# Optimization experiments

Hardware: AMD Instinct MI355X
Metric: run time of the kernel (lower is better)

## Reference

```python
import jax, jax.numpy as jnp
import numpy as np
from jax import lax

B, C, H, W = 16, 256, 56, 56
GROUPS = 4
K = 3
DILATIONS = (1, 3, 5)
EPS = 1e-5


@jax.custom_vjp
def bin_act(x):
    return jnp.sign(x)

def _bin_act_fwd(x):
    return jnp.sign(x), x

def _bin_act_bwd(x, g):
    grad = jnp.where((x >= -1.0) & (x <= 0.0), 2.0 + 2.0 * x, 0.0) \
         + jnp.where((x > 0.0) & (x <= 1.0), 2.0 - 2.0 * x, 0.0)
    return (grad * g,)

bin_act.defvjp(_bin_act_fwd, _bin_act_bwd)


def _bin_weight(wi):
    # per-output-channel scaling from raw |w|, centered sign, clip-STE
    scale = lax.stop_gradient(jnp.mean(jnp.abs(wi), axis=(1, 2, 3), keepdims=True))
    wc = wi - jnp.mean(wi, axis=(1, 2, 3), keepdims=True)
    clipped = jnp.clip(wc, -1.0, 1.0)
    return lax.stop_gradient(scale * jnp.sign(wc) - clipped) + clipped


def setup_inputs() -> dict:
    key = jax.random.key(0)
    ks = jax.random.split(key, 3)
    x = jax.random.normal(ks[0], (B, C, H, W), dtype=jnp.float32)
    # 3 branches of grouped conv weights: (3, C_out, C_in/groups, K, K)
    w = jax.random.normal(ks[1], (3, C, C // GROUPS, K, K), dtype=jnp.float32) * 0.05
    cb = jax.random.normal(ks[2], (3, C), dtype=jnp.float32) * 0.01
    return {
        "x": x,
        "bias": jnp.zeros((1, C, 1, 1), jnp.float32),   # LearnableBias
        "w": w,
        "cb": cb,                                        # conv biases
        "move1": jnp.zeros((3, C), jnp.float32),
        "alpha": jnp.full((3, C), 0.25, jnp.float32),    # PReLU slopes
        "move2": jnp.zeros((3, C), jnp.float32),
        "gamma": jnp.ones((C,), jnp.float32),            # LayerNorm weight
        "beta": jnp.zeros((C,), jnp.float32),            # LayerNorm bias
    }


def reference(x, bias, w, cb, move1, alpha, move2, gamma, beta):
    xb = x + bias
    xq = bin_act(xb)  # binarized activations, shared across branches
    out = jnp.zeros_like(x)
    for i, d in enumerate(DILATIONS):
        wq = _bin_weight(w[i])
        y = lax.conv_general_dilated(
            xq, wq,
            window_strides=(1, 1),
            padding=[(d, d), (d, d)],  # 'same' for k=3 with dilation d
            rhs_dilation=(d, d),
            dimension_numbers=("NCHW", "OIHW", "NCHW"),
            feature_group_count=GROUPS,
        )
        y = y + cb[i][None, :, None, None]
        # RPReLU: shift, channel-wise PReLU, shift
        y = y - move1[i][None, :, None, None]
        y = jnp.where(y >= 0, y, alpha[i][None, :, None, None] * y)
        y = y + move2[i][None, :, None, None]
        out = out + y
    # LayerNorm over channel dim (equivalent to NHWC last-dim LN)
    mean = jnp.mean(out, axis=1, keepdims=True)
    var = jnp.var(out, axis=1, keepdims=True)
    out = (out - mean) * lax.rsqrt(var + EPS)
    out = out * gamma[None, :, None, None] + beta[None, :, None, None]
    return out
```

## Files before the change

kernel.cpp:

```cpp
#include <hip/hip_runtime.h>
#include <hip/hip_fp16.h>
#include <stdint.h>

static constexpr int Bc = 16, Cc = 256, Hc = 56, Wc = 56, Gc = 4, CGc = 64;
static constexpr int HWc = Hc * Wc;
static constexpr float EPSc = 1e-5f;


static constexpr int SBS = 260;

__global__ __launch_bounds__(256) void k_prep(
    const float* __restrict__ w, const float* __restrict__ x,
    const float* __restrict__ bias, uint64_t* __restrict__ wbits,
    float* __restrict__ scales, uint64_t* __restrict__ abits,
    uint32_t* __restrict__ zero_area) {
  const int t = threadIdx.x;
  if (blockIdx.x < 192) {
    const int io = blockIdx.x * 4 + (t >> 6);
    const int i = io >> 8, o = io & 255;
    const int lane = t & 63;
    const float* wp = w + (size_t)io * 576 + lane * 9;
    float v[9];
    float ssum = 0.f, sabs = 0.f;
#pragma unroll
    for (int k = 0; k < 9; ++k) {
      v[k] = wp[k];
      ssum += v[k];
      sabs += fabsf(v[k]);
    }
#pragma unroll
    for (int off = 32; off > 0; off >>= 1) {
      ssum += __shfl_down(ssum, off);
      sabs += __shfl_down(sabs, off);
    }
    const float mean = __shfl(ssum, 0) * (1.f / 576.f);
    const float scale = __shfl(sabs, 0) * (1.f / 576.f);
#pragma unroll
    for (int k = 0; k < 9; ++k) {
      unsigned long long m = __ballot(v[k] > mean);
      if (lane == 0) wbits[(i * 9 + k) * Cc + o] = m;
    }
    if (lane == 0) scales[io] = scale;
  } else if (blockIdx.x == 192) {
    zero_area[t] = 0;
  } else {
    __shared__ uint8_t sb[Wc * SBS];
    const int bid = blockIdx.x - 193;
    const int b = bid / Hc, h = bid % Hc;
    const float* xb = x + ((size_t)b * Cc) * HWc + h * Wc;
#pragma unroll
    for (int k = 0; k < 14; ++k) {
      const int idx = k * 256 + t;
      const int c = idx / 14, q = idx - c * 14;
      const float4 v = *(const float4*)(xb + (size_t)c * HWc + q * 4);
      const float bc = bias[c];
      sb[(q * 4 + 0) * SBS + c] = (v.x + bc > 0.f);
      sb[(q * 4 + 1) * SBS + c] = (v.y + bc > 0.f);
      sb[(q * 4 + 2) * SBS + c] = (v.z + bc > 0.f);
      sb[(q * 4 + 3) * SBS + c] = (v.w + bc > 0.f);
    }
    __syncthreads();
    if (t < Gc * Wc) {
      const int g = t / Wc, ww = t - g * Wc;
      const uint32_t* p = (const uint32_t*)(sb + ww * SBS + g * 64);
      uint64_t word = 0;
#pragma unroll
      for (int dw = 0; dw < 16; ++dw) {
        const uint32_t d = p[dw];
        const uint32_t nib = (d | (d >> 7) | (d >> 14) | (d >> 21)) & 0xF;
        word |= (uint64_t)nib << (4 * dw);
      }
      abits[(((size_t)b * Gc + g) * Hc + h) * Wc + ww] = word;
    }
  }
}

template <int D>
struct Branch {
  uint64_t wgt[9];
  const uint64_t *r0, *r1, *r2;
  int BL, BM, BR;
  float sc, cbm1, al;

  __device__ __forceinline__ void init(const uint64_t* __restrict__ wb,
                                       const uint64_t* rowbase,
                                       const uint64_t* zrow, int h,
                                       float sc_, float cbm1_, float al_) {
    sc = sc_; cbm1 = cbm1_; al = al_;
    int z[9];
#pragma unroll
    for (int k = 0; k < 9; ++k) {
      wgt[k] = wb[k * Cc];
      z[k] = 64 - 2 * (int)__builtin_popcountll(wgt[k]);
    }
    const bool v0 = (h - D >= 0), v2 = (h + D < Hc);
    r0 = v0 ? (rowbase + (size_t)(h - D) * Wc) : zrow;
    r1 = rowbase + (size_t)h * Wc;
    r2 = v2 ? (rowbase + (size_t)(h + D) * Wc) : zrow;
    const int Z0 = (v0 ? 0 : z[0]) + (v2 ? 0 : z[6]);
    const int Z1 = (v0 ? 0 : z[1]) + (v2 ? 0 : z[7]);
    const int Z2 = (v0 ? 0 : z[2]) + (v2 ? 0 : z[8]);
    BM = 576 - Z0 - Z1 - Z2;
    BL = 384 - Z1 - Z2;
    BR = 384 - Z0 - Z1;
  }

  __device__ __forceinline__ void accum(int c0, int acc[14]) const {
#pragma unroll
    for (int kh = 0; kh < 3; ++kh) {
      const uint64_t* rp = (kh == 0) ? r0 : (kh == 1 ? r1 : r2);
      uint64_t sa[14 + 2 * D];
#pragma unroll
      for (int j = 0; j < 14 + 2 * D; ++j) sa[j] = rp[c0 - D + j];
#pragma unroll
      for (int ww = 0; ww < 14; ++ww) {
#pragma unroll
        for (int kw = 0; kw < 3; ++kw) {
          const int col = c0 + ww + D * (kw - 1);
          if (col < 0 || col >= Wc) continue;
          acc[ww] += (int)__builtin_popcountll(wgt[kh * 3 + kw] ^ sa[ww + D * kw]);
        }
      }
    }
  }

  __device__ __forceinline__ void epi(int c0, const int acc[14],
                                      float outf[14]) const {
#pragma unroll
    for (int ww = 0; ww < 14; ++ww) {
      const int wg = c0 + ww;
      const int B = (wg < D) ? BL : ((wg >= Wc - D) ? BR : BM);
      const float y0 = fmaf(sc, (float)(B - 2 * acc[ww]), cbm1);
      outf[ww] += fmaxf(y0, 0.f) + al * fminf(y0, 0.f);
    }
  }
};

static constexpr int TS2 = 58;

__global__ __launch_bounds__(256, 4) void k_conv_ln(
    const uint64_t* __restrict__ abits, const uint64_t* __restrict__ zrow,
    const uint64_t* __restrict__ wbits, const float* __restrict__ scales,
    const float* __restrict__ cb, const float* __restrict__ mv1,
    const float* __restrict__ al, const float* __restrict__ mv2,
    const float* __restrict__ gamma, const float* __restrict__ beta,
    float* __restrict__ out) {
  __shared__ __half out_tile[Cc * TS2];
  __shared__ float redu[4][Wc], redq[4][Wc];
  __shared__ float mstat[Wc], rstat[Wc];

  const int bid = blockIdx.x;
  const int b = bid / Hc, h = bid % Hc;
  const int t = threadIdx.x;
  const int gu = __builtin_amdgcn_readfirstlane(t >> 6);

  const uint64_t* rowbase = abits + ((size_t)b * Gc + gu) * Hc * Wc;

  Branch<1> b0; Branch<3> b1; Branch<5> b2;
  b0.init(wbits + 0 * 9 * Cc + t, rowbase, zrow, h, scales[0 * Cc + t],
          cb[0 * Cc + t] - mv1[0 * Cc + t], al[0 * Cc + t]);
  b1.init(wbits + 1 * 9 * Cc + t, rowbase, zrow, h, scales[1 * Cc + t],
          cb[1 * Cc + t] - mv1[1 * Cc + t], al[1 * Cc + t]);
  b2.init(wbits + 2 * 9 * Cc + t, rowbase, zrow, h, scales[2 * Cc + t],
          cb[2 * Cc + t] - mv1[2 * Cc + t], al[2 * Cc + t]);
  const float m2sum = mv2[0 * Cc + t] + mv2[1 * Cc + t] + mv2[2 * Cc + t];

#pragma unroll
  for (int ch = 0; ch < 4; ++ch) {
    const int c0 = ch * 14;
    float outf[14];
#pragma unroll
    for (int ww = 0; ww < 14; ++ww) outf[ww] = m2sum;
    { int acc[14] = {}; b0.accum(c0, acc); b0.epi(c0, acc, outf); }
    { int acc[14] = {}; b1.accum(c0, acc); b1.epi(c0, acc, outf); }
    { int acc[14] = {}; b2.accum(c0, acc); b2.epi(c0, acc, outf); }
#pragma unroll
    for (int ww = 0; ww < 14; ww += 2) {
      __half2 hv;
      hv.x = __float2half(outf[ww]);
      hv.y = __float2half(outf[ww + 1]);
      *(__half2*)&out_tile[t * TS2 + c0 + ww] = hv;
    }
  }
  __syncthreads();

  if (t < 4 * Wc) {
    const int ww = t % Wc;
    const int cq = t / Wc;
    float s = 0.f, sq = 0.f;
#pragma unroll 4
    for (int c = cq * 64; c < cq * 64 + 64; ++c) {
      const float v = __half2float(out_tile[c * TS2 + ww]);
      s += v;
      sq = fmaf(v, v, sq);
    }
    redu[cq][ww] = s;
    redq[cq][ww] = sq;
  }
  __syncthreads();
  if (t < Wc) {
    const float s = redu[0][t] + redu[1][t] + redu[2][t] + redu[3][t];
    const float sq = redq[0][t] + redq[1][t] + redq[2][t] + redq[3][t];
    const float mean = s * (1.f / 256.f);
    const float var = sq * (1.f / 256.f) - mean * mean;
    mstat[t] = mean;
    rstat[t] = rsqrtf(var + EPSc);
  }
  __syncthreads();

  float* base = out + ((size_t)b * Cc * Hc + h) * Wc;
  for (int idx = t; idx < Cc * Wc; idx += 256) {
    const int c = idx / Wc;
    const int ww = idx - c * Wc;
    const float v = __half2float(out_tile[c * TS2 + ww]);
    base[(size_t)c * HWc + ww] = (v - mstat[ww]) * rstat[ww] * gamma[c] + beta[c];
  }
}

extern "C" void kernel_launch(void* const* d_in, const int* in_sizes, int n_in,
                              void* d_out, int out_size, void* d_ws, size_t ws_size,
                              hipStream_t stream) {
  const float* x     = (const float*)d_in[0];
  const float* bias  = (const float*)d_in[1];
  const float* w     = (const float*)d_in[2];
  const float* cb    = (const float*)d_in[3];
  const float* mv1   = (const float*)d_in[4];
  const float* al    = (const float*)d_in[5];
  const float* mv2   = (const float*)d_in[6];
  const float* gamma = (const float*)d_in[7];
  const float* beta  = (const float*)d_in[8];
  float* out = (float*)d_out;

  uint8_t* ws = (uint8_t*)d_ws;
  uint32_t* zero_area = (uint32_t*)ws;
  const uint64_t* zrow = (const uint64_t*)(ws + 64);
  uint64_t* abits = (uint64_t*)(ws + 1024);
  uint64_t* wbits = (uint64_t*)(ws + 1024 + (size_t)200704 * 8);
  float* scales   = (float*)(ws + 1024 + (size_t)200704 * 8 + 6912 * 8);

  hipLaunchKernelGGL(k_prep, dim3(192 + 1 + Bc * Hc), dim3(256), 0, stream,
                     w, x, bias, wbits, scales, abits, zero_area);
  hipLaunchKernelGGL(k_conv_ln, dim3(Bc * Hc), dim3(256), 0, stream,
                     abits, zrow, wbits, scales, cb, mv1, al, mv2, gamma, beta,
                     out);
}
```

Before: 196.5 us.

## Pad bit-packed activation rows with zero columns and drop conv boundary branches

Activation bit rows are stored with a padded pitch of 72 words, with 8 zero words on each side, so the dilated 3x3 popcount conv can read neighbouring columns without checking column bounds. The width loop changes from 4 chunks of 14 to 7 chunks of 8, no longer fully unrolled. Left and right edge corrections are folded into per-pixel bias adjustments. This removes per-tap boundary branches and cuts register pressure, at the cost of a larger workspace, extra padding writes in the prep kernel and a redundant zero store.

```diff
diff --git a/kernel.cpp b/kernel.cpp
--- a/kernel.cpp
+++ b/kernel.cpp
@@ -5,6 +5,8 @@
 static constexpr int Bc = 16, Cc = 256, Hc = 56, Wc = 56, Gc = 4, CGc = 64;
 static constexpr int HWc = Hc * Wc;
 static constexpr float EPSc = 1e-5f;
+static constexpr int ROWP = 72;
+static constexpr int COL0 = 8;
 
 
 static constexpr int SBS = 260;
@@ -60,17 +62,24 @@
       sb[(q * 4 + 3) * SBS + c] = (v.w + bc > 0.f);
     }
     __syncthreads();
-    if (t < Gc * Wc) {
-      const int g = t / Wc, ww = t - g * Wc;
-      const uint32_t* p = (const uint32_t*)(sb + ww * SBS + g * 64);
+    for (int idx = t; idx < Gc * ROWP; idx += 256) {
+      const int g = idx / ROWP, k = idx - g * ROWP;
       uint64_t word = 0;
-#pragma unroll
-      for (int dw = 0; dw < 16; ++dw) {
-        const uint32_t d = p[dw];
-        const uint32_t nib = (d | (d >> 7) | (d >> 14) | (d >> 21)) & 0xF;
-        word |= (uint64_t)nib << (4 * dw);
+      if (k >= COL0 && k < COL0 + Wc) {
+        const int ww = k - COL0;
+        const uint32_t* p = (const uint32_t*)(sb + ww * SBS + g * 64);
+        uint64_t acc = 0;
+#pragma unroll
+        for (int dw = 0; dw < 16; ++dw) {
+          const uint32_t d = p[dw];
+          const uint32_t nib = (d | (d >> 7) | (d >> 14) | (d >> 21)) & 0xF;
+          acc |= (uint64_t)nib << (4 * dw);
+        }
+        word = acc;
       }
-      abits[(((size_t)b * Gc + g) * Hc + h) * Wc + ww] = word;
+      abits[(((size_t)b * Gc + g) * Hc + h) * ROWP + idx - g * ROWP +
+            (size_t)g * 0] = 0;
+      abits[(((size_t)b * Gc + g) * Hc + h) * ROWP + k] = word;
     }
   }
 }
@@ -79,12 +88,12 @@
 struct Branch {
   uint64_t wgt[9];
   const uint64_t *r0, *r1, *r2;
-  int BL, BM, BR;
+  int BM, ZL, ZR;
   float sc, cbm1, al;
 
   __device__ __forceinline__ void init(const uint64_t* __restrict__ wb,
                                        const uint64_t* rowbase,
-                                       const uint64_t* zrow, int h,
+                                       const uint64_t* zrowp, int h,
                                        float sc_, float cbm1_, float al_) {
     sc = sc_; cbm1 = cbm1_; al = al_;
     int z[9];
@@ -94,42 +103,39 @@
       z[k] = 64 - 2 * (int)__builtin_popcountll(wgt[k]);
     }
     const bool v0 = (h - D >= 0), v2 = (h + D < Hc);
-    r0 = v0 ? (rowbase + (size_t)(h - D) * Wc) : zrow;
-    r1 = rowbase + (size_t)h * Wc;
-    r2 = v2 ? (rowbase + (size_t)(h + D) * Wc) : zrow;
-    const int Z0 = (v0 ? 0 : z[0]) + (v2 ? 0 : z[6]);
-    const int Z1 = (v0 ? 0 : z[1]) + (v2 ? 0 : z[7]);
-    const int Z2 = (v0 ? 0 : z[2]) + (v2 ? 0 : z[8]);
-    BM = 576 - Z0 - Z1 - Z2;
-    BL = 384 - Z1 - Z2;
-    BR = 384 - Z0 - Z1;
-  }
-
-  __device__ __forceinline__ void accum(int c0, int acc[14]) const {
+    r0 = v0 ? (rowbase + (size_t)(h - D) * ROWP) : zrowp;
+    r1 = rowbase + (size_t)h * ROWP;
+    r2 = v2 ? (rowbase + (size_t)(h + D) * ROWP) : zrowp;
+    const int Zrow = (v0 ? 0 : (z[0] + z[1] + z[2])) +
+                     (v2 ? 0 : (z[6] + z[7] + z[8]));
+    BM = 576 - Zrow;
+    ZL = (v0 ? z[0] : 0) + z[3] + (v2 ? z[6] : 0);
+    ZR = (v0 ? z[2] : 0) + z[5] + (v2 ? z[8] : 0);
+  }
+
+  __device__ __forceinline__ void accum8(int w0, int acc[8]) const {
 #pragma unroll
     for (int kh = 0; kh < 3; ++kh) {
       const uint64_t* rp = (kh == 0) ? r0 : (kh == 1 ? r1 : r2);
-      uint64_t sa[14 + 2 * D];
-#pragma unroll
-      for (int j = 0; j < 14 + 2 * D; ++j) sa[j] = rp[c0 - D + j];
-#pragma unroll
-      for (int ww = 0; ww < 14; ++ww) {
-#pragma unroll
-        for (int kw = 0; kw < 3; ++kw) {
-          const int col = c0 + ww + D * (kw - 1);
-          if (col < 0 || col >= Wc) continue;
-          acc[ww] += (int)__builtin_popcountll(wgt[kh * 3 + kw] ^ sa[ww + D * kw]);
-        }
+      uint64_t seg[8 + 2 * D];
+#pragma unroll
+      for (int j = 0; j < 8 + 2 * D; ++j) seg[j] = rp[w0 - D + j];
+#pragma unroll
+      for (int ww = 0; ww < 8; ++ww) {
+#pragma unroll
+        for (int kw = 0; kw < 3; ++kw)
+          acc[ww] +=
+              (int)__builtin_popcountll(wgt[kh * 3 + kw] ^ seg[ww + D * kw]);
       }
     }
   }
 
-  __device__ __forceinline__ void epi(int c0, const int acc[14],
-                                      float outf[14]) const {
-#pragma unroll
-    for (int ww = 0; ww < 14; ++ww) {
-      const int wg = c0 + ww;
-      const int B = (wg < D) ? BL : ((wg >= Wc - D) ? BR : BM);
+  __device__ __forceinline__ void epi8(int w0, const int acc[8],
+                                       float outf[8]) const {
+#pragma unroll
+    for (int ww = 0; ww < 8; ++ww) {
+      const int w = w0 + ww;
+      const int B = BM - ((w < D) ? ZL : 0) - ((w >= Wc - D) ? ZR : 0);
       const float y0 = fmaf(sc, (float)(B - 2 * acc[ww]), cbm1);
       outf[ww] += fmaxf(y0, 0.f) + al * fminf(y0, 0.f);
     }
@@ -139,7 +145,7 @@
 static constexpr int TS2 = 58;
 
 __global__ __launch_bounds__(256, 4) void k_conv_ln(
-    const uint64_t* __restrict__ abits, const uint64_t* __restrict__ zrow,
+    const uint64_t* __restrict__ abits, const uint64_t* __restrict__ zrowp,
     const uint64_t* __restrict__ wbits, const float* __restrict__ scales,
     const float* __restrict__ cb, const float* __restrict__ mv1,
     const float* __restrict__ al, const float* __restrict__ mv2,
@@ -154,32 +160,31 @@
   const int t = threadIdx.x;
   const int gu = __builtin_amdgcn_readfirstlane(t >> 6);
 
-  const uint64_t* rowbase = abits + ((size_t)b * Gc + gu) * Hc * Wc;
+  const uint64_t* rowbase = abits + ((size_t)b * Gc + gu) * Hc * ROWP + COL0;
 
   Branch<1> b0; Branch<3> b1; Branch<5> b2;
-  b0.init(wbits + 0 * 9 * Cc + t, rowbase, zrow, h, scales[0 * Cc + t],
+  b0.init(wbits + 0 * 9 * Cc + t, rowbase, zrowp, h, scales[0 * Cc + t],
           cb[0 * Cc + t] - mv1[0 * Cc + t], al[0 * Cc + t]);
-  b1.init(wbits + 1 * 9 * Cc + t, rowbase, zrow, h, scales[1 * Cc + t],
+  b1.init(wbits + 1 * 9 * Cc + t, rowbase, zrowp, h, scales[1 * Cc + t],
           cb[1 * Cc + t] - mv1[1 * Cc + t], al[1 * Cc + t]);
-  b2.init(wbits + 2 * 9 * Cc + t, rowbase, zrow, h, scales[2 * Cc + t],
+  b2.init(wbits + 2 * 9 * Cc + t, rowbase, zrowp, h, scales[2 * Cc + t],
           cb[2 * Cc + t] - mv1[2 * Cc + t], al[2 * Cc + t]);
   const float m2sum = mv2[0 * Cc + t] + mv2[1 * Cc + t] + mv2[2 * Cc + t];
 
-#pragma unroll
-  for (int ch = 0; ch < 4; ++ch) {
-    const int c0 = ch * 14;
-    float outf[14];
-#pragma unroll
-    for (int ww = 0; ww < 14; ++ww) outf[ww] = m2sum;
-    { int acc[14] = {}; b0.accum(c0, acc); b0.epi(c0, acc, outf); }
-    { int acc[14] = {}; b1.accum(c0, acc); b1.epi(c0, acc, outf); }
-    { int acc[14] = {}; b2.accum(c0, acc); b2.epi(c0, acc, outf); }
-#pragma unroll
-    for (int ww = 0; ww < 14; ww += 2) {
+  for (int ch = 0; ch < 7; ++ch) {
+    const int w0 = ch * 8;
+    float outf[8];
+#pragma unroll
+    for (int ww = 0; ww < 8; ++ww) outf[ww] = m2sum;
+    { int acc[8] = {}; b0.accum8(w0, acc); b0.epi8(w0, acc, outf); }
+    { int acc[8] = {}; b1.accum8(w0, acc); b1.epi8(w0, acc, outf); }
+    { int acc[8] = {}; b2.accum8(w0, acc); b2.epi8(w0, acc, outf); }
+#pragma unroll
+    for (int ww = 0; ww < 8; ww += 2) {
       __half2 hv;
       hv.x = __float2half(outf[ww]);
       hv.y = __float2half(outf[ww + 1]);
-      *(__half2*)&out_tile[t * TS2 + c0 + ww] = hv;
+      *(__half2*)&out_tile[t * TS2 + w0 + ww] = hv;
     }
   }
   __syncthreads();
@@ -233,14 +238,15 @@
 
   uint8_t* ws = (uint8_t*)d_ws;
   uint32_t* zero_area = (uint32_t*)ws;
-  const uint64_t* zrow = (const uint64_t*)(ws + 64);
+  const uint64_t* zrowp = (const uint64_t*)ws + COL0;
   uint64_t* abits = (uint64_t*)(ws + 1024);
-  uint64_t* wbits = (uint64_t*)(ws + 1024 + (size_t)200704 * 8);
-  float* scales   = (float*)(ws + 1024 + (size_t)200704 * 8 + 6912 * 8);
+  const size_t abits_bytes = (size_t)Bc * Gc * Hc * ROWP * 8;
+  uint64_t* wbits = (uint64_t*)(ws + 1024 + abits_bytes);
+  float* scales = (float*)(ws + 1024 + abits_bytes + 6912 * 8);
 
   hipLaunchKernelGGL(k_prep, dim3(192 + 1 + Bc * Hc), dim3(256), 0, stream,
                      w, x, bias, wbits, scales, abits, zero_area);
   hipLaunchKernelGGL(k_conv_ln, dim3(Bc * Hc), dim3(256), 0, stream,
-                     abits, zrow, wbits, scales, cb, mv1, al, mv2, gamma, beta,
+                     abits, zrowp, wbits, scales, cb, mv1, al, mv2, gamma, beta,
                      out);
 }
```

New measurement: 186.7 us. -5.0%, faster.
